# Performance work log

Measured on AMD Instinct MI355X. Metric: run time of the kernel, lower is better.

Reference implementation:

```python
import jax, jax.numpy as jnp
import numpy as np
from jax import lax

B, C, T_IN = 512, 22, 1001   # input width includes the subject-id column
K, KS, P = 40, 25, 100       # num_kernels, kernel_size, pool_size
S, NOUT = 9, 4               # num_subjects, n_outputs
BN_EPS = 1e-5


def setup_inputs() -> dict:
    key = jax.random.key(0)
    ks = jax.random.split(key, 6)
    x = jax.random.normal(ks[0], (B, C, T_IN), dtype=jnp.float32)
    # subject ids in 1..9 encoded as id*1e6 at x[:, 0, -1] (as in the torch module)
    sid = jax.random.randint(ks[1], (B,), 1, S + 1)
    x = x.at[:, 0, -1].set(sid.astype(jnp.float32) * 1e6)
    W = 0.05 * jax.random.normal(ks[2], (S, K, C, KS), dtype=jnp.float32)
    b = 0.05 * jax.random.normal(ks[3], (S, K), dtype=jnp.float32)
    gamma = jnp.ones((K,), dtype=jnp.float32)
    beta = jnp.zeros((K,), dtype=jnp.float32)
    fc_in = K * ((T_IN - 1 - KS + 1) // P)  # 40 * 9 = 360
    fc_w = 0.05 * jax.random.normal(ks[4], (NOUT, fc_in), dtype=jnp.float32)
    fc_b = jnp.zeros((NOUT,), dtype=jnp.float32)
    return {"x": x, "W": W, "b": b, "gamma": gamma, "beta": beta,
            "fc_w": fc_w, "fc_b": fc_b}


def reference(x, W, b, gamma, beta, fc_w, fc_b):
    # decode per-sample subject routing id (0-based into stacked weights)
    sid = (x[:, 0, -1] / 1e6).astype(jnp.int32) - 1        # [B]
    xs = x[:, :, :-1]                                      # [B, C, T]
    Wg = W[sid]                                            # [B, K, C, KS] gathered expert weights
    bg = b[sid]                                            # [B, K]

    # per-sample 1D valid conv with its own expert weights (batched via vmap)
    def conv1(xi, wi):  # xi: [C, T], wi: [K, C, KS]
        return lax.conv_general_dilated(xi[None], wi, (1,), 'VALID',
                                        dimension_numbers=('NCH', 'OIH', 'NCH'))[0]

    y = jax.vmap(conv1)(xs, Wg) + bg[:, :, None]           # [B, K, To]
    y = jax.nn.elu(y)

    # BatchNorm2d in training mode: batch statistics over (B, spatial), biased var
    mean = y.mean(axis=(0, 2))
    var = y.var(axis=(0, 2))
    y = (y - mean[None, :, None]) * (gamma / jnp.sqrt(var + BN_EPS))[None, :, None] \
        + beta[None, :, None]

    # AvgPool over non-overlapping windows of size P (stride = P, floor)
    To = y.shape[-1]
    nw = To // P
    y = y[..., : nw * P].reshape(y.shape[0], K, nw, P).mean(axis=-1)  # [B, K, nw]

    y = y.reshape(y.shape[0], -1)          # [B, K*nw]; dropout is identity in eval
    return y @ fc_w.T + fc_b               # [B, NOUT]
```

## Files before the change

kernel.cpp:

```cpp
#include <hip/hip_runtime.h>
#include <hip/hip_bf16.h>

#define B_ 512
#define C_ 22
#define TIN 1001
#define K_ 40
#define KS_ 25
#define TO 976
#define P_ 100
#define NW 9
#define NOUT 4
#define FCIN 360

#define XTROWS 1088
#define QR 272
#define SROWS 320
#define STG_BYTES (SROWS * 64)
#define RED_OFF STG_BYTES
#define RED_BYTES (K_ * 4 * 2 * 4)
#define LDS_TOTAL (RED_OFF + RED_BYTES)
#define NBLKQ 2048
#define NPAD 48
#define WB_ELEM_S (KS_ * NPAD * 32)

typedef __attribute__((ext_vector_type(8))) short bf16x8;
typedef __attribute__((ext_vector_type(4))) float f32x4;
typedef __attribute__((ext_vector_type(4))) int i32x4;

__device__ __forceinline__ float waveReduceSum(float v) {
#pragma unroll
  for (int m = 32; m >= 1; m >>= 1) v += __shfl_xor(v, m, 64);
  return v;
}

__device__ __forceinline__ unsigned short f2bf(float f) {
  __hip_bfloat16 h = __float2bfloat16(f);
  return *reinterpret_cast<unsigned short*>(&h);
}

__device__ __forceinline__ void gll16(const void* g, void* l) {
  __builtin_amdgcn_global_load_lds(
      (const __attribute__((address_space(1))) unsigned int*)g,
      (__attribute__((address_space(3))) unsigned int*)l, 16, 0, 0);
}

__global__ __launch_bounds__(192) void wconv_kernel(const float* __restrict__ W,
                                                    unsigned short* __restrict__ WBg) {
  const int s = blockIdx.x / KS_;
  const int j = blockIdx.x % KS_;
  const int n = threadIdx.x >> 2;
  const int q = threadIdx.x & 3;
  union {
    unsigned short u[8];
    i32x4 v;
  } pk;
#pragma unroll
  for (int e = 0; e < 8; ++e) {
    const int c = q * 8 + e;
    float v = 0.f;
    if (n < K_ && c < C_) v = W[(((size_t)s * K_ + n) * C_ + c) * KS_ + j];
    pk.u[e] = f2bf(v);
  }
  *(i32x4*)(WBg + ((size_t)(s * KS_ + j) * NPAD + n) * 32 + q * 8) = pk.v;
}

__global__ __launch_bounds__(256) void xpose_kernel(const float* __restrict__ x,
                                                    unsigned short* __restrict__ XTg) {
  const int blk = blockIdx.x;
  const int b = blk >> 2;
  const int p = blk & 3;
  const float* xb = x + (size_t)b * (C_ * TIN);
  unsigned short* xt = XTg + ((size_t)b * XTROWS + p * QR) * 32;
#pragma unroll
  for (int r = 0; r < 5; ++r) {
    const int task = threadIdx.x + r * 256;
    if (task < 4 * QR) {
      const int trl = task >> 2;
      const int q = task & 3;
      const int tr = p * QR + trl;
      const int lq = q ^ ((tr >> 1) & 3);
      union {
        unsigned short u[8];
        i32x4 v;
      } pk;
#pragma unroll
      for (int e = 0; e < 8; ++e) {
        const int c = lq * 8 + e;
        float v = 0.f;
        if (c < C_ && tr < TIN - 1) v = xb[c * TIN + tr];
        pk.u[e] = f2bf(v);
      }
      *(i32x4*)(xt + (size_t)trl * 32 + q * 8) = pk.v;
    }
  }
}

#define MFMA12(A, Bv)                                                          \
  do {                                                                         \
    _Pragma("unroll") for (int nt_ = 0; nt_ < 3; ++nt_) {                      \
      _Pragma("unroll") for (int m_ = 0; m_ < 4; ++m_) {                       \
        acc[m_][nt_] =                                                         \
            __builtin_amdgcn_mfma_f32_16x16x32_bf16(A[m_], Bv[nt_], acc[m_][nt_], 0, 0, 0); \
      }                                                                        \
    }                                                                          \
  } while (0)

#define LDA(J, A)                                                              \
  do {                                                                         \
    const int tl_ = tbl + (J);                                                 \
    const char* ap_ = sm + tl_ * 64 + ((lg ^ ((tl_ >> 1) & 3)) << 4);          \
    _Pragma("unroll") for (int m_ = 0; m_ < 4; ++m_) {                         \
      A[m_] = *(const bf16x8*)(ap_ + m_ * 1024);                               \
    }                                                                          \
  } while (0)

#define LDB(J, Bv)                                                             \
  do {                                                                         \
    const unsigned short* bp_ = WBs + (J) * 1536;                              \
    _Pragma("unroll") for (int nt_ = 0; nt_ < 3; ++nt_) {                      \
      Bv[nt_] = *(const bf16x8*)(bp_ + nt_ * 512);                             \
    }                                                                          \
  } while (0)

__global__ __launch_bounds__(256, 3) void conv_kernel(
    const unsigned short* __restrict__ XTg, const unsigned short* __restrict__ WBg,
    const float* __restrict__ x, const float* __restrict__ bias,
    float* __restrict__ pooled, float* __restrict__ part_sum,
    float* __restrict__ part_sq) {
  extern __shared__ __align__(16) char sm[];
  const int blk = blockIdx.x;
  const int b = blk >> 2;
  const int p = blk & 3;
  const int rbg = p * 256;
  const int tid = threadIdx.x;

  int s = (int)rintf(x[(size_t)b * (C_ * TIN) + (TIN - 1)] * 1e-6f) - 1;
  s = __builtin_amdgcn_readfirstlane(min(max(s, 0), 8));

  {
    const char* src = (const char*)XTg + ((size_t)b * XTROWS + rbg) * 64;
#pragma unroll
    for (int r = 0; r < 5; ++r) {
      const int i = tid + r * 256;
      gll16(src + i * 16, sm + i * 16);
    }
  }
  __syncthreads();

  const int lane = tid & 63;
  const int wv = tid >> 6;
  const int l15 = lane & 15;
  const int lg = lane >> 4;
  const int tbl = wv * 64 + l15;

  const unsigned short* WBs = WBg + (size_t)s * WB_ELEM_S + (l15 * 32 + lg * 8);

  f32x4 acc[4][3];
#pragma unroll
  for (int m = 0; m < 4; ++m)
#pragma unroll
    for (int nt = 0; nt < 3; ++nt) acc[m][nt] = (f32x4){0.f, 0.f, 0.f, 0.f};

  bf16x8 Aa[3][4];
  bf16x8 Bb[4][3];

  LDA(0, Aa[0]);
  LDA(1, Aa[1]);
  LDB(0, Bb[0]);
  LDB(1, Bb[1]);
  LDB(2, Bb[2]);

#pragma unroll
  for (int j = 0; j <= 24; ++j) {
    if (j + 2 <= 24) LDA(j + 2, Aa[(j + 2) % 3]);
    if (j + 3 <= 24) LDB(j + 3, Bb[(j + 3) & 3]);
    MFMA12(Aa[j % 3], Bb[j & 3]);
  }

  float bv[3];
#pragma unroll
  for (int nt = 0; nt < 3; ++nt) {
    const int k = nt * 16 + l15;
    bv[nt] = bias[s * K_ + (k < K_ ? k : 0)];
  }
  const int wbase = rbg / P_;
  const int base100 = wbase * P_;
  float sY[3] = {0.f, 0.f, 0.f}, sY2[3] = {0.f, 0.f, 0.f};
  float pw[4][3];
#pragma unroll
  for (int w4 = 0; w4 < 4; ++w4)
#pragma unroll
    for (int nt = 0; nt < 3; ++nt) pw[w4][nt] = 0.f;

#pragma unroll
  for (int m = 0; m < 4; ++m) {
#pragma unroll
    for (int i = 0; i < 4; ++i) {
      const int t = rbg + wv * 64 + m * 16 + lg * 4 + i;
      const bool valid = (t < TO);
      const bool pool = (t < NW * P_);
      const int d = t - base100;
#pragma unroll
      for (int nt = 0; nt < 3; ++nt) {
        const float v = acc[m][nt][i] + bv[nt];
        const float y = v > 0.f ? v : (__expf(v) - 1.f);
        if (valid) {
          sY[nt] += y;
          sY2[nt] = fmaf(y, y, sY2[nt]);
          if (pool) {
            if (d < P_)
              pw[0][nt] += y;
            else if (d < 2 * P_)
              pw[1][nt] += y;
            else if (d < 3 * P_)
              pw[2][nt] += y;
            else
              pw[3][nt] += y;
          }
        }
      }
    }
  }

  float* red = (float*)(sm + RED_OFF);
#pragma unroll
  for (int nt = 0; nt < 3; ++nt) {
#pragma unroll
    for (int r = 16; r <= 32; r <<= 1) {
      pw[0][nt] += __shfl_xor(pw[0][nt], r, 64);
      pw[1][nt] += __shfl_xor(pw[1][nt], r, 64);
      pw[2][nt] += __shfl_xor(pw[2][nt], r, 64);
      pw[3][nt] += __shfl_xor(pw[3][nt], r, 64);
      sY[nt] += __shfl_xor(sY[nt], r, 64);
      sY2[nt] += __shfl_xor(sY2[nt], r, 64);
    }
    const int k = nt * 16 + l15;
    if (lane < 16 && k < K_) {
      float* pb = pooled + (size_t)b * FCIN + k * NW;
#pragma unroll
      for (int w4 = 0; w4 < 4; ++w4) {
        const int wg = wbase + w4;
        if (wg <= NW - 1 && pw[w4][nt] != 0.f) atomicAdd(&pb[wg], pw[w4][nt]);
      }
      red[k * 4 + wv] = sY[nt];
      red[K_ * 4 + k * 4 + wv] = sY2[nt];
    }
  }
  __syncthreads();
  if (tid < K_) {
    float a = 0.f, q = 0.f;
#pragma unroll
    for (int i = 0; i < 4; ++i) {
      a += red[tid * 4 + i];
      q += red[K_ * 4 + tid * 4 + i];
    }
    part_sum[(size_t)tid * NBLKQ + blk] = a;
    part_sq[(size_t)tid * NBLKQ + blk] = q;
  }
}

__global__ __launch_bounds__(256) void stats_kernel(
    const float* __restrict__ part_sum, const float* __restrict__ part_sq,
    const float* __restrict__ gamma, const float* __restrict__ beta,
    float* __restrict__ ss) {
  const int k = blockIdx.x;
  float s = 0.f, q = 0.f;
  for (int i = threadIdx.x; i < NBLKQ; i += 256) {
    s += part_sum[(size_t)k * NBLKQ + i];
    q += part_sq[(size_t)k * NBLKQ + i];
  }
  s = waveReduceSum(s);
  q = waveReduceSum(q);
  __shared__ float ls[4], lq[4];
  const int wave = threadIdx.x >> 6, lane = threadIdx.x & 63;
  if (lane == 0) {
    ls[wave] = s;
    lq[wave] = q;
  }
  __syncthreads();
  if (threadIdx.x == 0) {
    const float S = ls[0] + ls[1] + ls[2] + ls[3];
    const float Q = lq[0] + lq[1] + lq[2] + lq[3];
    const float N = (float)B_ * (float)TO;
    const float mean = S / N;
    const float var = Q / N - mean * mean;
    const float sc = gamma[k] / sqrtf(var + 1e-5f);
    ss[k] = sc;
    ss[K_ + k] = beta[k] - mean * sc;
  }
}

__global__ __launch_bounds__(256) void fc_kernel(
    const float* __restrict__ pooled, const float* __restrict__ ss,
    const float* __restrict__ fc_w, const float* __restrict__ fc_b,
    float* __restrict__ out) {
  const int bb = blockIdx.x;
  const int n = threadIdx.x >> 6;
  const int lane = threadIdx.x & 63;
  float acc = 0.f;
  for (int i = lane; i < FCIN; i += 64) {
    const int k = i / NW;
    const float y = pooled[(size_t)bb * FCIN + i] * (1.f / (float)P_) * ss[k] + ss[K_ + k];
    acc = fmaf(y, fc_w[n * FCIN + i], acc);
  }
  acc = waveReduceSum(acc);
  if (lane == 0) out[bb * NOUT + n] = acc + fc_b[n];
}

extern "C" void kernel_launch(void* const* d_in, const int* in_sizes, int n_in,
                              void* d_out, int out_size, void* d_ws, size_t ws_size,
                              hipStream_t stream) {
  const float* x = (const float*)d_in[0];
  const float* W = (const float*)d_in[1];
  const float* bias = (const float*)d_in[2];
  const float* gamma = (const float*)d_in[3];
  const float* beta = (const float*)d_in[4];
  const float* fc_w = (const float*)d_in[5];
  const float* fc_b = (const float*)d_in[6];
  float* out = (float*)d_out;

  char* ws = (char*)d_ws;
  float* pooled = (float*)ws;
  float* part_sum = (float*)(ws + 737280);
  float* part_sq = (float*)(ws + 1064960);
  unsigned short* WBg = (unsigned short*)(ws + 1392640);
  float* ss = (float*)(ws + 2083840);
  unsigned short* XTg = (unsigned short*)(ws + 2084160);

  (void)hipFuncSetAttribute((const void*)conv_kernel,
                            hipFuncAttributeMaxDynamicSharedMemorySize, LDS_TOTAL);

  (void)hipMemsetAsync(pooled, 0, 737280, stream);
  wconv_kernel<<<9 * KS_, 192, 0, stream>>>(W, WBg);
  xpose_kernel<<<NBLKQ, 256, 0, stream>>>(x, XTg);
  conv_kernel<<<NBLKQ, 256, LDS_TOTAL, stream>>>(XTg, WBg, x, bias, pooled,
                                                 part_sum, part_sq);
  stats_kernel<<<K_, 256, 0, stream>>>(part_sum, part_sq, gamma, beta, ss);
  fc_kernel<<<B_, 256, 0, stream>>>(pooled, ss, fc_w, fc_b, out);
}
```

Measured before the change: 100.3 us.

## Pack conv reduction into contiguous 24-channel rows to cut padded MFMA steps

Each transposed input row now holds 24 bf16 channels (48 bytes) instead of 32. The reduction over (tap, channel) is flattened into 19 contiguous 32-wide K chunks instead of 25 per-tap chunks, which removes most of the zero-padding MFMA work and shrinks the LDS staging and transposed buffer. The XOR swizzle is dropped, the register pipeline depth drops to double buffering, and occupancy is raised to 4 blocks per CU. The unswizzled 48-byte row stride may cause LDS bank conflicts, and the shallower prefetch may expose more load latency.

New measurement: 107.0 us. 6.7% more time.

```diff
diff --git a/kernel.cpp b/kernel.cpp
--- a/kernel.cpp
+++ b/kernel.cpp
@@ -12,16 +12,20 @@
 #define NOUT 4
 #define FCIN 360
 
-#define XTROWS 1088
-#define QR 272
-#define SROWS 320
-#define STG_BYTES (SROWS * 64)
+#define ROWE 24
+#define ROWB 48
+#define KCH 19
+#define XTROWS 1056
+#define SROWS 288
+#define STG_BYTES (SROWS * ROWB)
+#define STG_CH (STG_BYTES / 16)
 #define RED_OFF STG_BYTES
 #define RED_BYTES (K_ * 4 * 2 * 4)
 #define LDS_TOTAL (RED_OFF + RED_BYTES)
 #define NBLKQ 2048
 #define NPAD 48
-#define WB_ELEM_S (KS_ * NPAD * 32)
+#define WB_ELEM_S (KCH * NPAD * 32)
+#define XQR 264
 
 typedef __attribute__((ext_vector_type(8))) short bf16x8;
 typedef __attribute__((ext_vector_type(4))) float f32x4;
@@ -46,22 +50,24 @@
 
 __global__ __launch_bounds__(192) void wconv_kernel(const float* __restrict__ W,
                                                     unsigned short* __restrict__ WBg) {
-  const int s = blockIdx.x / KS_;
-  const int j = blockIdx.x % KS_;
+  const int s = blockIdx.x / KCH;
+  const int kk = blockIdx.x % KCH;
   const int n = threadIdx.x >> 2;
-  const int q = threadIdx.x & 3;
+  const int lg = threadIdx.x & 3;
   union {
     unsigned short u[8];
     i32x4 v;
   } pk;
 #pragma unroll
   for (int e = 0; e < 8; ++e) {
-    const int c = q * 8 + e;
+    const int r = kk * 32 + lg * 8 + e;
+    const int j = r / ROWE;
+    const int c = r - j * ROWE;
     float v = 0.f;
-    if (n < K_ && c < C_) v = W[(((size_t)s * K_ + n) * C_ + c) * KS_ + j];
+    if (n < K_ && c < C_ && j < KS_) v = W[(((size_t)s * K_ + n) * C_ + c) * KS_ + j];
     pk.u[e] = f2bf(v);
   }
-  *(i32x4*)(WBg + ((size_t)(s * KS_ + j) * NPAD + n) * 32 + q * 8) = pk.v;
+  *(i32x4*)(WBg + ((size_t)(s * KCH + kk) * NPAD + n) * 32 + lg * 8) = pk.v;
 }
 
 __global__ __launch_bounds__(256) void xpose_kernel(const float* __restrict__ x,
@@ -70,27 +76,26 @@
   const int b = blk >> 2;
   const int p = blk & 3;
   const float* xb = x + (size_t)b * (C_ * TIN);
-  unsigned short* xt = XTg + ((size_t)b * XTROWS + p * QR) * 32;
-#pragma unroll
-  for (int r = 0; r < 5; ++r) {
+  unsigned short* xt = XTg + ((size_t)b * XTROWS + p * XQR) * ROWE;
+#pragma unroll
+  for (int r = 0; r < 4; ++r) {
     const int task = threadIdx.x + r * 256;
-    if (task < 4 * QR) {
-      const int trl = task >> 2;
-      const int q = task & 3;
-      const int tr = p * QR + trl;
-      const int lq = q ^ ((tr >> 1) & 3);
+    if (task < 3 * XQR) {
+      const int trl = task / 3;
+      const int q = task - trl * 3;
+      const int tr = p * XQR + trl;
       union {
         unsigned short u[8];
         i32x4 v;
       } pk;
 #pragma unroll
       for (int e = 0; e < 8; ++e) {
-        const int c = lq * 8 + e;
+        const int c = q * 8 + e;
         float v = 0.f;
         if (c < C_ && tr < TIN - 1) v = xb[c * TIN + tr];
         pk.u[e] = f2bf(v);
       }
-      *(i32x4*)(xt + (size_t)trl * 32 + q * 8) = pk.v;
+      *(i32x4*)(xt + (size_t)trl * ROWE + q * 8) = pk.v;
     }
   }
 }
@@ -105,24 +110,23 @@
     }                                                                          \
   } while (0)
 
-#define LDA(J, A)                                                              \
+#define LDA(KK, A)                                                             \
   do {                                                                         \
-    const int tl_ = tbl + (J);                                                 \
-    const char* ap_ = sm + tl_ * 64 + ((lg ^ ((tl_ >> 1) & 3)) << 4);          \
+    const char* ap_ = abase + (KK) * 64;                                       \
     _Pragma("unroll") for (int m_ = 0; m_ < 4; ++m_) {                         \
-      A[m_] = *(const bf16x8*)(ap_ + m_ * 1024);                               \
+      A[m_] = *(const bf16x8*)(ap_ + m_ * 768);                                \
     }                                                                          \
   } while (0)
 
-#define LDB(J, Bv)                                                             \
+#define LDB(KK, Bv)                                                            \
   do {                                                                         \
-    const unsigned short* bp_ = WBs + (J) * 1536;                              \
+    const unsigned short* bp_ = WBs + (KK) * 1536;                             \
     _Pragma("unroll") for (int nt_ = 0; nt_ < 3; ++nt_) {                      \
       Bv[nt_] = *(const bf16x8*)(bp_ + nt_ * 512);                             \
     }                                                                          \
   } while (0)
 
-__global__ __launch_bounds__(256, 3) void conv_kernel(
+__global__ __launch_bounds__(256, 4) void conv_kernel(
     const unsigned short* __restrict__ XTg, const unsigned short* __restrict__ WBg,
     const float* __restrict__ x, const float* __restrict__ bias,
     float* __restrict__ pooled, float* __restrict__ part_sum,
@@ -138,11 +142,11 @@
   s = __builtin_amdgcn_readfirstlane(min(max(s, 0), 8));
 
   {
-    const char* src = (const char*)XTg + ((size_t)b * XTROWS + rbg) * 64;
-#pragma unroll
-    for (int r = 0; r < 5; ++r) {
+    const char* src = (const char*)XTg + ((size_t)b * XTROWS + rbg) * ROWB;
+#pragma unroll
+    for (int r = 0; r < 4; ++r) {
       const int i = tid + r * 256;
-      gll16(src + i * 16, sm + i * 16);
+      if (i < STG_CH) gll16(src + i * 16, sm + i * 16);
     }
   }
   __syncthreads();
@@ -152,6 +156,7 @@
   const int l15 = lane & 15;
   const int lg = lane >> 4;
   const int tbl = wv * 64 + l15;
+  const char* abase = sm + tbl * ROWB + lg * 16;
 
   const unsigned short* WBs = WBg + (size_t)s * WB_ELEM_S + (l15 * 32 + lg * 8);
 
@@ -161,20 +166,18 @@
 #pragma unroll
     for (int nt = 0; nt < 3; ++nt) acc[m][nt] = (f32x4){0.f, 0.f, 0.f, 0.f};
 
-  bf16x8 Aa[3][4];
-  bf16x8 Bb[4][3];
+  bf16x8 Aa[2][4];
+  bf16x8 Bb[2][3];
 
   LDA(0, Aa[0]);
-  LDA(1, Aa[1]);
   LDB(0, Bb[0]);
-  LDB(1, Bb[1]);
-  LDB(2, Bb[2]);
-
-#pragma unroll
-  for (int j = 0; j <= 24; ++j) {
-    if (j + 2 <= 24) LDA(j + 2, Aa[(j + 2) % 3]);
-    if (j + 3 <= 24) LDB(j + 3, Bb[(j + 3) & 3]);
-    MFMA12(Aa[j % 3], Bb[j & 3]);
+#pragma unroll
+  for (int kk = 0; kk < KCH; ++kk) {
+    if (kk + 1 < KCH) {
+      LDA(kk + 1, Aa[(kk + 1) & 1]);
+      LDB(kk + 1, Bb[(kk + 1) & 1]);
+    }
+    MFMA12(Aa[kk & 1], Bb[kk & 1]);
   }
 
   float bv[3];
@@ -324,14 +327,14 @@
   float* part_sum = (float*)(ws + 737280);
   float* part_sq = (float*)(ws + 1064960);
   unsigned short* WBg = (unsigned short*)(ws + 1392640);
-  float* ss = (float*)(ws + 2083840);
-  unsigned short* XTg = (unsigned short*)(ws + 2084160);
+  float* ss = (float*)(ws + 1917952);
+  unsigned short* XTg = (unsigned short*)(ws + 1918272);
 
   (void)hipFuncSetAttribute((const void*)conv_kernel,
                             hipFuncAttributeMaxDynamicSharedMemorySize, LDS_TOTAL);
 
   (void)hipMemsetAsync(pooled, 0, 737280, stream);
-  wconv_kernel<<<9 * KS_, 192, 0, stream>>>(W, WBg);
+  wconv_kernel<<<9 * KCH, 192, 0, stream>>>(W, WBg);
   xpose_kernel<<<NBLKQ, 256, 0, stream>>>(x, XTg);
   conv_kernel<<<NBLKQ, 256, LDS_TOTAL, stream>>>(XTg, WBg, x, bias, pooled,
                                                  part_sum, part_sq);
```
